# Kernel tuning notes

Measured on AMD Instinct MI355X. Metric: run time of the kernel, lower is better.

## Reference

```python
import jax, jax.numpy as jnp
import numpy as np

BETA_2 = 1.0
LAMBDA_2 = 1.0


def _segment_logsumexp(x, seg, num_segments):
    # numerically stable segment logsumexp; empty segments -> 0.0
    m = jax.ops.segment_max(x, seg, num_segments=num_segments)
    m_safe = jnp.where(jnp.isfinite(m), m, 0.0)
    s = jax.ops.segment_sum(jnp.exp(x - m_safe[seg]), seg, num_segments=num_segments)
    lse = m_safe + jnp.log(s)
    return jnp.where(s > 0, lse, 0.0)


def setup_inputs() -> dict:
    key = jax.random.key(0)
    k1, k2, k3, k4, k5 = jax.random.split(key, 5)
    num_nodes, d, num_edges, num_graphs = 100000, 64, 3200000, 256
    Q2 = jax.random.normal(k1, (num_nodes, d), dtype=jnp.float32)
    K2 = jax.random.normal(k2, (num_nodes, d), dtype=jnp.float32)
    c_2 = jax.random.randint(k3, (num_edges,), 0, num_nodes)
    u_2 = jax.random.randint(k4, (num_edges,), 0, num_nodes)
    batch = jnp.sort(jax.random.randint(k5, (num_nodes,), 0, num_graphs))
    return {"Q2": Q2, "K2": K2, "c_2": c_2, "u_2": u_2, "batch": batch,
            "num_graphs": num_graphs}


def reference(Q2, K2, c_2, u_2, batch, num_graphs):
    num_nodes, d = Q2.shape
    scale = d ** 0.5
    # pairwise dot over edges: [E]
    ell_2 = jnp.sum(Q2[c_2] * K2[u_2], axis=-1) / scale
    # segment logsumexp grouped by destination node c: [N]
    lse_2 = _segment_logsumexp(BETA_2 * ell_2, c_2, num_nodes)
    # scatter-add per-node lse into per-graph energy: [G]
    graph_lse = jax.ops.segment_sum(lse_2, batch, num_segments=num_graphs)
    E = (LAMBDA_2 / BETA_2) * graph_lse
    return E
```

## Files before the change

kernel.cpp:

```cpp
#include <hip/hip_runtime.h>
#include <hip/hip_fp8.h>
#include <math.h>

typedef __attribute__((ext_vector_type(2))) float fv2;

#if defined(__has_builtin)
#  if __has_builtin(__builtin_amdgcn_cvt_pk_f32_fp8) && \
      __has_builtin(__builtin_amdgcn_cvt_pk_fp8_f32)
#    define PE_HAVE_FP8_BUILTINS 1
#  endif
#endif

#define MAX_NB 1024
#define NPB 256
#define NPB_SHIFT 8
#define B2_EPT 16
#define B2_CHUNK (B2_EPT * 256)
#define CPB 4
#define RT 1024
#define NXCD 8

__device__ __forceinline__ unsigned pack4_fp8(float a, float b, float c, float d) {
#ifdef PE_HAVE_FP8_BUILTINS
    int w = 0;
    w = __builtin_amdgcn_cvt_pk_fp8_f32(a, b, w, false);
    w = __builtin_amdgcn_cvt_pk_fp8_f32(c, d, w, true);
    return (unsigned)w;
#else
    unsigned r = 0;
    r |= (unsigned)__hip_fp8_e4m3(a).__x;
    r |= (unsigned)__hip_fp8_e4m3(b).__x << 8;
    r |= (unsigned)__hip_fp8_e4m3(c).__x << 16;
    r |= (unsigned)__hip_fp8_e4m3(d).__x << 24;
    return r;
#endif
}

__device__ __forceinline__ float dot4w_fp8(unsigned qa, unsigned ka, float acc) {
#ifdef PE_HAVE_FP8_BUILTINS
    fv2 q0 = __builtin_amdgcn_cvt_pk_f32_fp8((int)qa, false);
    fv2 q1 = __builtin_amdgcn_cvt_pk_f32_fp8((int)qa, true);
    fv2 k0 = __builtin_amdgcn_cvt_pk_f32_fp8((int)ka, false);
    fv2 k1 = __builtin_amdgcn_cvt_pk_f32_fp8((int)ka, true);
    acc = fmaf(q0.x, k0.x, acc);
    acc = fmaf(q0.y, k0.y, acc);
    acc = fmaf(q1.x, k1.x, acc);
    acc = fmaf(q1.y, k1.y, acc);
    return acc;
#else
#pragma unroll
    for (int j = 0; j < 4; ++j) {
        __hip_fp8_e4m3 qv, kv;
        qv.__x = (qa >> (8 * j)) & 0xff;
        kv.__x = (ka >> (8 * j)) & 0xff;
        acc = fmaf((float)qv, (float)kv, acc);
    }
    return acc;
#endif
}

__device__ __forceinline__ float dot16_fp8(const uint4& q, const uint4& k) {
    float d = 0.0f;
    d = dot4w_fp8(q.x, k.x, d);
    d = dot4w_fp8(q.y, k.y, d);
    d = dot4w_fp8(q.z, k.z, d);
    d = dot4w_fp8(q.w, k.w, d);
    return d;
}

__device__ __forceinline__ float red4(float d) {
    d += __shfl_xor(d, 1, 64);
    d += __shfl_xor(d, 2, 64);
    return d;
}

__global__ __launch_bounds__(256) void pe_convert_kernel(
    const float* __restrict__ Q,
    const float* __restrict__ K,
    unsigned* __restrict__ Qq,
    unsigned* __restrict__ Kq,
    float* __restrict__ node_sum,
    float* __restrict__ out,
    int n4,
    int num_nodes,
    int num_graphs) {
    const int i = blockIdx.x * blockDim.x + threadIdx.x;
    if (i < num_nodes) node_sum[i] = 0.0f;
    if (i < num_graphs) out[i] = 0.0f;
    if (i >= n4) return;

    const float4 q = ((const float4*)Q)[i];
    const float4 k = ((const float4*)K)[i];
    Qq[i] = pack4_fp8(q.x, q.y, q.z, q.w);
    Kq[i] = pack4_fp8(k.x, k.y, k.z, k.w);
}

__global__ __launch_bounds__(256) void pe_count_kernel(
    const int* __restrict__ c,
    unsigned* __restrict__ cnt_mat,
    int num_edges, int nb, int nblk) {
    __shared__ unsigned h[MAX_NB];
    const int tid = threadIdx.x;
    const int blk = blockIdx.x;
    for (int b = tid; b < nb; b += 256) h[b] = 0u;
    __syncthreads();

    const int estart = blk * B2_CHUNK;
    const int ecount = min(B2_CHUNK, num_edges - estart);
    const int n4 = ecount >> 2;
    const int4* c4 = (const int4*)(c + estart);
    for (int k = tid; k < n4; k += 256) {
        const int4 v = c4[k];
        atomicAdd(&h[v.x >> NPB_SHIFT], 1u);
        atomicAdd(&h[v.y >> NPB_SHIFT], 1u);
        atomicAdd(&h[v.z >> NPB_SHIFT], 1u);
        atomicAdd(&h[v.w >> NPB_SHIFT], 1u);
    }
    for (int e = (n4 << 2) + tid; e < ecount; e += 256)
        atomicAdd(&h[c[estart + e] >> NPB_SHIFT], 1u);
    __syncthreads();

    for (int b = tid; b < nb; b += 256)
        cnt_mat[(size_t)b * nblk + blk] = h[b];
}

__global__ __launch_bounds__(256) void pe_matscan_kernel(
    unsigned* __restrict__ cnt_mat,
    unsigned* __restrict__ bucket_cnt,
    int nblk) {
    __shared__ unsigned s[256];
    const int t = threadIdx.x;
    unsigned* row = cnt_mat + (size_t)blockIdx.x * nblk;
    unsigned carry = 0u;
    for (int t0 = 0; t0 < nblk; t0 += 256) {
        const int i = t0 + t;
        const unsigned v = (i < nblk) ? row[i] : 0u;
        s[t] = v;
        __syncthreads();
        for (int off = 1; off < 256; off <<= 1) {
            const unsigned mine = s[t];
            const unsigned add = (t >= off) ? s[t - off] : 0u;
            __syncthreads();
            s[t] = mine + add;
            __syncthreads();
        }
        if (i < nblk) row[i] = carry + (s[t] - v);
        carry += s[255];
        __syncthreads();
    }
    if (t == 0) bucket_cnt[blockIdx.x] = carry;
}

__global__ __launch_bounds__(1024) void pe_scan_kernel(
    const unsigned* __restrict__ bucket_cnt,
    unsigned* __restrict__ bucket_base,
    int nb) {
    __shared__ unsigned s[MAX_NB];
    const int t = threadIdx.x;
    const unsigned v = (t < nb) ? bucket_cnt[t] : 0u;
    s[t] = v;
    __syncthreads();
    for (int off = 1; off < MAX_NB; off <<= 1) {
        const unsigned mine = s[t];
        const unsigned add = (t >= off) ? s[t - off] : 0u;
        __syncthreads();
        s[t] = mine + add;
        __syncthreads();
    }
    if (t < nb) bucket_base[t] = s[t] - v;
    if (t == 0) bucket_base[nb] = s[MAX_NB - 1];
}

__global__ __launch_bounds__(256) void pe_binify_kernel(
    const int* __restrict__ c,
    const int* __restrict__ u,
    const unsigned* __restrict__ cnt_mat,
    const unsigned* __restrict__ bucket_base,
    unsigned* __restrict__ recs,
    int num_edges, int nb, int nblk) {
    __shared__ unsigned rank[MAX_NB];
    __shared__ unsigned lstart[MAX_NB];
    __shared__ unsigned basesh[MAX_NB];
    __shared__ unsigned srec[B2_CHUNK];
    __shared__ unsigned short sbuk[B2_CHUNK];
    __shared__ unsigned wtot[4];

    const int tid = threadIdx.x;
    const int blk = blockIdx.x;
    const int estart = blk * B2_CHUNK;
    const int ecount = min(B2_CHUNK, num_edges - estart);

    for (int b = tid; b < MAX_NB; b += 256) rank[b] = 0u;
    for (int b = tid; b < nb; b += 256)
        basesh[b] = bucket_base[b] + cnt_mat[(size_t)b * nblk + blk];
    __syncthreads();

    unsigned rw[B2_EPT];
    int rb[B2_EPT];
    unsigned rr[B2_EPT];

    if (ecount == B2_CHUNK) {
        const int4* c4 = (const int4*)(c + estart);
        const int4* u4 = (const int4*)(u + estart);
#pragma unroll
        for (int jj = 0; jj < 4; ++jj) {
            const int k = jj * 256 + tid;
            const int4 cv = c4[k];
            const int4 uv = u4[k];
            const int j = jj * 4;
            rb[j + 0] = cv.x >> NPB_SHIFT;
            rb[j + 1] = cv.y >> NPB_SHIFT;
            rb[j + 2] = cv.z >> NPB_SHIFT;
            rb[j + 3] = cv.w >> NPB_SHIFT;
            rw[j + 0] = ((unsigned)uv.x << NPB_SHIFT) | (unsigned)(cv.x & (NPB - 1));
            rw[j + 1] = ((unsigned)uv.y << NPB_SHIFT) | (unsigned)(cv.y & (NPB - 1));
            rw[j + 2] = ((unsigned)uv.z << NPB_SHIFT) | (unsigned)(cv.z & (NPB - 1));
            rw[j + 3] = ((unsigned)uv.w << NPB_SHIFT) | (unsigned)(cv.w & (NPB - 1));
            rr[j + 0] = atomicAdd(&rank[rb[j + 0]], 1u);
            rr[j + 1] = atomicAdd(&rank[rb[j + 1]], 1u);
            rr[j + 2] = atomicAdd(&rank[rb[j + 2]], 1u);
            rr[j + 3] = atomicAdd(&rank[rb[j + 3]], 1u);
        }
    } else {
#pragma unroll
        for (int j = 0; j < B2_EPT; ++j) {
            rb[j] = -1;
            const int e = estart + j * 256 + tid;
            if (e < num_edges) {
                const int cc = c[e];
                const int uu = u[e];
                rb[j] = cc >> NPB_SHIFT;
                rw[j] = ((unsigned)uu << NPB_SHIFT) | (unsigned)(cc & (NPB - 1));
                rr[j] = atomicAdd(&rank[rb[j]], 1u);
            }
        }
    }
    __syncthreads();

    {
        const int b4 = tid * 4;
        const unsigned v0 = rank[b4 + 0];
        const unsigned v1 = rank[b4 + 1];
        const unsigned v2 = rank[b4 + 2];
        const unsigned v3 = rank[b4 + 3];
        const unsigned tsum = v0 + v1 + v2 + v3;
        unsigned incl = tsum;
        const int lane = tid & 63;
#pragma unroll
        for (int off = 1; off < 64; off <<= 1) {
            const unsigned nv = __shfl_up(incl, off, 64);
            if (lane >= off) incl += nv;
        }
        if (lane == 63) wtot[tid >> 6] = incl;
        __syncthreads();
        unsigned woff = 0;
        const int w = tid >> 6;
        for (int i = 0; i < w; ++i) woff += wtot[i];
        const unsigned ebase = woff + incl - tsum;
        lstart[b4 + 0] = ebase;
        lstart[b4 + 1] = ebase + v0;
        lstart[b4 + 2] = ebase + v0 + v1;
        lstart[b4 + 3] = ebase + v0 + v1 + v2;
    }
    __syncthreads();

#pragma unroll
    for (int j = 0; j < B2_EPT; ++j) {
        if (rb[j] >= 0) {
            const unsigned pos = lstart[rb[j]] + rr[j];
            srec[pos] = rw[j];
            sbuk[pos] = (unsigned short)rb[j];
        }
    }
    __syncthreads();

    for (int i = tid; i < ecount; i += 256) {
        const int b = sbuk[i];
        recs[basesh[b] + (unsigned)i - lstart[b]] = srec[i];
    }
}

__global__ __launch_bounds__(256) void pe_dotred_kernel(
    const unsigned* __restrict__ Qq,
    const unsigned* __restrict__ Kq,
    const unsigned* __restrict__ recs,
    const unsigned* __restrict__ bucket_base,
    float* __restrict__ node_sum,
    int num_nodes, int nb) {
    __shared__ uint4 qlds[NPB * 4];
    __shared__ float acc[NPB];
    __shared__ unsigned rlds[RT];

    const int g = blockIdx.x;
    const int xcd = g & (NXCD - 1);
    const int slot = g >> 3;
    const int B = xcd + NXCD * (slot / CPB);
    const int chunk = slot - (slot / CPB) * CPB;
    if (B >= nb) return;

    const int t = threadIdx.x;
    const int gteam = t >> 2;
    const int sub = t & 3;
    const float inv_scale = 0.125f;

    const int nrows = min(NPB, num_nodes - B * NPB);
    const uint4* qsrc = (const uint4*)Qq + (size_t)B * NPB * 4;
    for (int i = t; i < nrows * 4; i += 256) qlds[i] = qsrc[i];
    acc[t] = 0.0f;

    const unsigned s0 = bucket_base[B];
    const unsigned len = bucket_base[B + 1] - s0;
    const unsigned r0 = s0 + (unsigned)(((unsigned long long)len * chunk) / CPB);
    const unsigned r1 = s0 + (unsigned)(((unsigned long long)len * (chunk + 1)) / CPB);

    for (unsigned t0 = r0; t0 < r1; t0 += RT) {
        const unsigned n = min((unsigned)RT, r1 - t0);
        __syncthreads();
        for (unsigned i = t; i < n; i += 256) rlds[i] = recs[t0 + i];
        __syncthreads();
        for (unsigned i = gteam; i < n; i += 64) {
            const unsigned rec = rlds[i];
            const unsigned uu = rec >> NPB_SHIFT;
            const unsigned local = rec & (NPB - 1);
            const uint4 k = *(const uint4*)(Kq + (size_t)uu * 16 + sub * 4);
            const uint4 q = qlds[local * 4 + sub];
            const float d = red4(dot16_fp8(q, k));
            if (sub == 0) atomicAdd(&acc[local], __expf(d * inv_scale));
        }
    }
    __syncthreads();

    if (t < nrows && acc[t] != 0.0f)
        atomicAdd(&node_sum[B * NPB + t], acc[t]);
}

__global__ __launch_bounds__(256) void pe_node_kernel(
    const float* __restrict__ node_sum,
    const int* __restrict__ batch,
    float* __restrict__ out,
    int num_nodes) {
    const int n = blockIdx.x * blockDim.x + threadIdx.x;
    const bool valid = (n < num_nodes);
    const int nc = valid ? n : (num_nodes - 1);

    const float s = valid ? node_sum[nc] : 0.0f;
    float lse = (s > 0.0f) ? logf(s) : 0.0f;
    if (!valid) lse = 0.0f;
    const int b = batch[nc];

    const int b0 = __shfl(b, 0, 64);
    const bool uniform = __all(b == b0);
    if (uniform) {
        lse += __shfl_xor(lse, 1, 64);
        lse += __shfl_xor(lse, 2, 64);
        lse += __shfl_xor(lse, 4, 64);
        lse += __shfl_xor(lse, 8, 64);
        lse += __shfl_xor(lse, 16, 64);
        lse += __shfl_xor(lse, 32, 64);
        if ((threadIdx.x & 63) == 0 && lse != 0.0f) {
            atomicAdd(&out[b0], lse);
        }
    } else {
        if (valid && lse != 0.0f) {
            atomicAdd(&out[b], lse);
        }
    }
}


__global__ __launch_bounds__(256) void pe_edge_kernel(
    const unsigned* __restrict__ Qq,
    const unsigned* __restrict__ Kq,
    const int* __restrict__ c,
    const int* __restrict__ u,
    float* __restrict__ node_sum,
    int num_edges) {
    const int tid = blockIdx.x * blockDim.x + threadIdx.x;
    const int group = tid >> 2;
    const int sub = tid & 3;
    const int ngroups = (gridDim.x * blockDim.x) >> 2;
    const float inv_scale = 0.125f;

    const int E4 = num_edges & ~3;

    for (int base = group * 4; base < E4; base += ngroups * 4) {
        const int4 ci = *(const int4*)(c + base);
        const int4 ui = *(const int4*)(u + base);

        const uint4 q0 = *(const uint4*)(Qq + (size_t)ci.x * 16 + sub * 4);
        const uint4 q1 = *(const uint4*)(Qq + (size_t)ci.y * 16 + sub * 4);
        const uint4 q2 = *(const uint4*)(Qq + (size_t)ci.z * 16 + sub * 4);
        const uint4 q3 = *(const uint4*)(Qq + (size_t)ci.w * 16 + sub * 4);
        const uint4 k0 = *(const uint4*)(Kq + (size_t)ui.x * 16 + sub * 4);
        const uint4 k1 = *(const uint4*)(Kq + (size_t)ui.y * 16 + sub * 4);
        const uint4 k2 = *(const uint4*)(Kq + (size_t)ui.z * 16 + sub * 4);
        const uint4 k3 = *(const uint4*)(Kq + (size_t)ui.w * 16 + sub * 4);

        float d0 = red4(dot16_fp8(q0, k0));
        float d1 = red4(dot16_fp8(q1, k1));
        float d2 = red4(dot16_fp8(q2, k2));
        float d3 = red4(dot16_fp8(q3, k3));

        const float dsel = (sub == 0) ? d0 : (sub == 1) ? d1 : (sub == 2) ? d2 : d3;
        const int csel = (sub == 0) ? ci.x : (sub == 1) ? ci.y : (sub == 2) ? ci.z : ci.w;
        atomicAdd(&node_sum[csel], __expf(dsel * inv_scale));
    }

    for (int e = E4 + group; e < num_edges; e += ngroups) {
        const int cc = c[e];
        const int uu = u[e];
        const uint4 q = *(const uint4*)(Qq + (size_t)cc * 16 + sub * 4);
        const uint4 k = *(const uint4*)(Kq + (size_t)uu * 16 + sub * 4);
        float d = red4(dot16_fp8(q, k));
        if (sub == 0) atomicAdd(&node_sum[cc], __expf(d * inv_scale));
    }
}

extern "C" void kernel_launch(void* const* d_in, const int* in_sizes, int n_in,
                              void* d_out, int out_size, void* d_ws, size_t ws_size,
                              hipStream_t stream) {
    const float* Q2 = (const float*)d_in[0];
    const float* K2 = (const float*)d_in[1];
    const int* c_2 = (const int*)d_in[2];
    const int* u_2 = (const int*)d_in[3];
    const int* batch = (const int*)d_in[4];

    const int num_nodes = in_sizes[4];
    const int num_edges = in_sizes[2];
    const int num_graphs = out_size;
    const int d = in_sizes[0] / num_nodes;
    const size_t row_elems = (size_t)num_nodes * d;
    const size_t row_bytes = row_elems;

    const int nb = (num_nodes + NPB - 1) >> NPB_SHIFT;
    const int nblk = (num_edges + B2_CHUNK - 1) / B2_CHUNK;

    unsigned* Qq = (unsigned*)d_ws;
    unsigned* Kq = Qq + row_bytes / 4;
    unsigned* meta = Kq + row_bytes / 4;
    unsigned* bucket_cnt = meta;
    unsigned* bucket_base = meta + MAX_NB;
    float* node_sum_b = (float*)(meta + 2 * MAX_NB + 16);
    const size_t ns_pad = ((size_t)num_nodes + 15) & ~(size_t)15;
    unsigned* recs = (unsigned*)node_sum_b + ns_pad;
    unsigned* cnt_mat = recs + num_edges;
    float* node_sum_f = (float*)meta;
    float* out = (float*)d_out;

    const size_t need_binned = row_bytes * 2 + (size_t)(2 * MAX_NB + 16) * 4 +
                               ns_pad * 4 + (size_t)num_edges * 4 +
                               (size_t)nb * nblk * 4;
    const bool use_binned = (nb <= MAX_NB) && (ws_size >= need_binned) &&
                            (d == 64) && (num_nodes <= (1 << 23));

    float* node_sum = use_binned ? node_sum_b : node_sum_f;

    {
        const int n4 = (int)(row_elems / 4);
        const int block = 256;
        const int grid = (n4 + block - 1) / block;
        pe_convert_kernel<<<grid, block, 0, stream>>>(
            Q2, K2, Qq, Kq, node_sum, out, n4, num_nodes, num_graphs);
    }

    if (use_binned) {
        pe_count_kernel<<<nblk, 256, 0, stream>>>(c_2, cnt_mat,
                                                  num_edges, nb, nblk);
        pe_matscan_kernel<<<nb, 256, 0, stream>>>(cnt_mat, bucket_cnt, nblk);
        pe_scan_kernel<<<1, 1024, 0, stream>>>(bucket_cnt, bucket_base, nb);
        pe_binify_kernel<<<nblk, 256, 0, stream>>>(c_2, u_2, cnt_mat,
                                                   bucket_base, recs,
                                                   num_edges, nb, nblk);
        {
            const int grid = NXCD * ((nb + NXCD - 1) / NXCD) * CPB;
            pe_dotred_kernel<<<grid, 256, 0, stream>>>(Qq, Kq, recs,
                                                       bucket_base,
                                                       node_sum, num_nodes, nb);
        }
    } else {
        pe_edge_kernel<<<8192, 256, 0, stream>>>(Qq, Kq, c_2, u_2,
                                                 node_sum, num_edges);
    }

    {
        const int block = 256;
        const int grid = (num_nodes + block - 1) / block;
        pe_node_kernel<<<grid, block, 0, stream>>>(node_sum, batch, out,
                                                   num_nodes);
    }
}
```

Measured before the change: 197.8 us.

## Sub-bin edges by source-node quarter and fuse convert with count kernel

Each destination bucket is split into four sub-bins by which quarter of the node range the source index u falls in. Within a bucket, the dot-product kernel then walks edges grouped by u range, which should improve cache locality of K row gathers. The FP8 conversion and the histogram count are merged into one launch, with block index deciding the role, to save a kernel launch and let the two overlap. In exchange the count matrix, scans and binify shared arrays get four times more bins, adding scan and shared-memory cost.

```diff
diff --git a/kernel.cpp b/kernel.cpp
--- a/kernel.cpp
+++ b/kernel.cpp
@@ -11,7 +11,9 @@
 #  endif
 #endif
 
-#define MAX_NB 1024
+#define MAX_NB 512
+#define MAX_NB2 2048
+#define UQ 4
 #define NPB 256
 #define NPB_SHIFT 8
 #define B2_EPT 16
@@ -74,59 +76,69 @@
     return d;
 }
 
-__global__ __launch_bounds__(256) void pe_convert_kernel(
+__device__ __forceinline__ int uquarter(int uu, int t1, int t2, int t3) {
+    return (uu >= t1) + (uu >= t2) + (uu >= t3);
+}
+
+__global__ __launch_bounds__(256) void pe_convcount_kernel(
     const float* __restrict__ Q,
     const float* __restrict__ K,
     unsigned* __restrict__ Qq,
     unsigned* __restrict__ Kq,
     float* __restrict__ node_sum,
     float* __restrict__ out,
-    int n4,
-    int num_nodes,
-    int num_graphs) {
-    const int i = blockIdx.x * blockDim.x + threadIdx.x;
-    if (i < num_nodes) node_sum[i] = 0.0f;
-    if (i < num_graphs) out[i] = 0.0f;
-    if (i >= n4) return;
-
-    const float4 q = ((const float4*)Q)[i];
-    const float4 k = ((const float4*)K)[i];
-    Qq[i] = pack4_fp8(q.x, q.y, q.z, q.w);
-    Kq[i] = pack4_fp8(k.x, k.y, k.z, k.w);
-}
-
-__global__ __launch_bounds__(256) void pe_count_kernel(
     const int* __restrict__ c,
+    const int* __restrict__ u,
     unsigned* __restrict__ cnt_mat,
-    int num_edges, int nb, int nblk) {
-    __shared__ unsigned h[MAX_NB];
+    int n4, int num_nodes, int num_graphs, int num_edges,
+    int nb2, int nblk, int nconv,
+    int t1, int t2, int t3) {
+    __shared__ unsigned h[MAX_NB2];
     const int tid = threadIdx.x;
-    const int blk = blockIdx.x;
-    for (int b = tid; b < nb; b += 256) h[b] = 0u;
+
+    if (blockIdx.x < nconv) {
+        const int i = blockIdx.x * 256 + tid;
+        if (i < num_nodes) node_sum[i] = 0.0f;
+        if (i < num_graphs) out[i] = 0.0f;
+        if (i >= n4) return;
+        const float4 q = ((const float4*)Q)[i];
+        const float4 k = ((const float4*)K)[i];
+        Qq[i] = pack4_fp8(q.x, q.y, q.z, q.w);
+        Kq[i] = pack4_fp8(k.x, k.y, k.z, k.w);
+        return;
+    }
+
+    const int blk = blockIdx.x - nconv;
+    for (int b = tid; b < nb2; b += 256) h[b] = 0u;
     __syncthreads();
 
     const int estart = blk * B2_CHUNK;
     const int ecount = min(B2_CHUNK, num_edges - estart);
-    const int n4 = ecount >> 2;
+    const int n4e = ecount >> 2;
     const int4* c4 = (const int4*)(c + estart);
-    for (int k = tid; k < n4; k += 256) {
-        const int4 v = c4[k];
-        atomicAdd(&h[v.x >> NPB_SHIFT], 1u);
-        atomicAdd(&h[v.y >> NPB_SHIFT], 1u);
-        atomicAdd(&h[v.z >> NPB_SHIFT], 1u);
-        atomicAdd(&h[v.w >> NPB_SHIFT], 1u);
-    }
-    for (int e = (n4 << 2) + tid; e < ecount; e += 256)
-        atomicAdd(&h[c[estart + e] >> NPB_SHIFT], 1u);
-    __syncthreads();
-
-    for (int b = tid; b < nb; b += 256)
+    const int4* u4 = (const int4*)(u + estart);
+    for (int k = tid; k < n4e; k += 256) {
+        const int4 cv = c4[k];
+        const int4 uv = u4[k];
+        atomicAdd(&h[(cv.x >> NPB_SHIFT) * UQ + uquarter(uv.x, t1, t2, t3)], 1u);
+        atomicAdd(&h[(cv.y >> NPB_SHIFT) * UQ + uquarter(uv.y, t1, t2, t3)], 1u);
+        atomicAdd(&h[(cv.z >> NPB_SHIFT) * UQ + uquarter(uv.z, t1, t2, t3)], 1u);
+        atomicAdd(&h[(cv.w >> NPB_SHIFT) * UQ + uquarter(uv.w, t1, t2, t3)], 1u);
+    }
+    for (int e = (n4e << 2) + tid; e < ecount; e += 256) {
+        const int cc = c[estart + e];
+        const int uu = u[estart + e];
+        atomicAdd(&h[(cc >> NPB_SHIFT) * UQ + uquarter(uu, t1, t2, t3)], 1u);
+    }
+    __syncthreads();
+
+    for (int b = tid; b < nb2; b += 256)
         cnt_mat[(size_t)b * nblk + blk] = h[b];
 }
 
 __global__ __launch_bounds__(256) void pe_matscan_kernel(
     unsigned* __restrict__ cnt_mat,
-    unsigned* __restrict__ bucket_cnt,
+    unsigned* __restrict__ bin_cnt,
     int nblk) {
     __shared__ unsigned s[256];
     const int t = threadIdx.x;
@@ -148,39 +160,45 @@
         carry += s[255];
         __syncthreads();
     }
-    if (t == 0) bucket_cnt[blockIdx.x] = carry;
+    if (t == 0) bin_cnt[blockIdx.x] = carry;
 }
 
 __global__ __launch_bounds__(1024) void pe_scan_kernel(
-    const unsigned* __restrict__ bucket_cnt,
-    unsigned* __restrict__ bucket_base,
-    int nb) {
-    __shared__ unsigned s[MAX_NB];
+    const unsigned* __restrict__ bin_cnt,
+    unsigned* __restrict__ bin_base,
+    int nb2) {
+    __shared__ unsigned s[1024];
     const int t = threadIdx.x;
-    const unsigned v = (t < nb) ? bucket_cnt[t] : 0u;
-    s[t] = v;
-    __syncthreads();
-    for (int off = 1; off < MAX_NB; off <<= 1) {
+    const int i0 = 2 * t, i1 = 2 * t + 1;
+    const unsigned v0 = (i0 < nb2) ? bin_cnt[i0] : 0u;
+    const unsigned v1 = (i1 < nb2) ? bin_cnt[i1] : 0u;
+    const unsigned p = v0 + v1;
+    s[t] = p;
+    __syncthreads();
+    for (int off = 1; off < 1024; off <<= 1) {
         const unsigned mine = s[t];
         const unsigned add = (t >= off) ? s[t - off] : 0u;
         __syncthreads();
         s[t] = mine + add;
         __syncthreads();
     }
-    if (t < nb) bucket_base[t] = s[t] - v;
-    if (t == 0) bucket_base[nb] = s[MAX_NB - 1];
+    const unsigned excl = s[t] - p;
+    if (i0 < nb2) bin_base[i0] = excl;
+    if (i1 < nb2) bin_base[i1] = excl + v0;
+    if (t == 1023) bin_base[nb2] = s[1023];
 }
 
 __global__ __launch_bounds__(256) void pe_binify_kernel(
     const int* __restrict__ c,
     const int* __restrict__ u,
     const unsigned* __restrict__ cnt_mat,
-    const unsigned* __restrict__ bucket_base,
+    const unsigned* __restrict__ bin_base,
     unsigned* __restrict__ recs,
-    int num_edges, int nb, int nblk) {
-    __shared__ unsigned rank[MAX_NB];
-    __shared__ unsigned lstart[MAX_NB];
-    __shared__ unsigned basesh[MAX_NB];
+    int num_edges, int nb2, int nblk,
+    int t1, int t2, int t3) {
+    __shared__ unsigned rank[MAX_NB2];
+    __shared__ unsigned lstart[MAX_NB2];
+    __shared__ unsigned basesh[MAX_NB2];
     __shared__ unsigned srec[B2_CHUNK];
     __shared__ unsigned short sbuk[B2_CHUNK];
     __shared__ unsigned wtot[4];
@@ -190,9 +208,9 @@
     const int estart = blk * B2_CHUNK;
     const int ecount = min(B2_CHUNK, num_edges - estart);
 
-    for (int b = tid; b < MAX_NB; b += 256) rank[b] = 0u;
-    for (int b = tid; b < nb; b += 256)
-        basesh[b] = bucket_base[b] + cnt_mat[(size_t)b * nblk + blk];
+    for (int b = tid; b < MAX_NB2; b += 256) rank[b] = 0u;
+    for (int b = tid; b < nb2; b += 256)
+        basesh[b] = bin_base[b] + cnt_mat[(size_t)b * nblk + blk];
     __syncthreads();
 
     unsigned rw[B2_EPT];
@@ -208,10 +226,10 @@
             const int4 cv = c4[k];
             const int4 uv = u4[k];
             const int j = jj * 4;
-            rb[j + 0] = cv.x >> NPB_SHIFT;
-            rb[j + 1] = cv.y >> NPB_SHIFT;
-            rb[j + 2] = cv.z >> NPB_SHIFT;
-            rb[j + 3] = cv.w >> NPB_SHIFT;
+            rb[j + 0] = (cv.x >> NPB_SHIFT) * UQ + uquarter(uv.x, t1, t2, t3);
+            rb[j + 1] = (cv.y >> NPB_SHIFT) * UQ + uquarter(uv.y, t1, t2, t3);
+            rb[j + 2] = (cv.z >> NPB_SHIFT) * UQ + uquarter(uv.z, t1, t2, t3);
+            rb[j + 3] = (cv.w >> NPB_SHIFT) * UQ + uquarter(uv.w, t1, t2, t3);
             rw[j + 0] = ((unsigned)uv.x << NPB_SHIFT) | (unsigned)(cv.x & (NPB - 1));
             rw[j + 1] = ((unsigned)uv.y << NPB_SHIFT) | (unsigned)(cv.y & (NPB - 1));
             rw[j + 2] = ((unsigned)uv.z << NPB_SHIFT) | (unsigned)(cv.z & (NPB - 1));
@@ -229,7 +247,7 @@
             if (e < num_edges) {
                 const int cc = c[e];
                 const int uu = u[e];
-                rb[j] = cc >> NPB_SHIFT;
+                rb[j] = (cc >> NPB_SHIFT) * UQ + uquarter(uu, t1, t2, t3);
                 rw[j] = ((unsigned)uu << NPB_SHIFT) | (unsigned)(cc & (NPB - 1));
                 rr[j] = atomicAdd(&rank[rb[j]], 1u);
             }
@@ -238,12 +256,11 @@
     __syncthreads();
 
     {
-        const int b4 = tid * 4;
-        const unsigned v0 = rank[b4 + 0];
-        const unsigned v1 = rank[b4 + 1];
-        const unsigned v2 = rank[b4 + 2];
-        const unsigned v3 = rank[b4 + 3];
-        const unsigned tsum = v0 + v1 + v2 + v3;
+        const int b8 = tid * 8;
+        unsigned v[8];
+        unsigned tsum = 0;
+#pragma unroll
+        for (int i = 0; i < 8; ++i) { v[i] = rank[b8 + i]; tsum += v[i]; }
         unsigned incl = tsum;
         const int lane = tid & 63;
 #pragma unroll
@@ -256,11 +273,9 @@
         unsigned woff = 0;
         const int w = tid >> 6;
         for (int i = 0; i < w; ++i) woff += wtot[i];
-        const unsigned ebase = woff + incl - tsum;
-        lstart[b4 + 0] = ebase;
-        lstart[b4 + 1] = ebase + v0;
-        lstart[b4 + 2] = ebase + v0 + v1;
-        lstart[b4 + 3] = ebase + v0 + v1 + v2;
+        unsigned run = woff + incl - tsum;
+#pragma unroll
+        for (int i = 0; i < 8; ++i) { lstart[b8 + i] = run; run += v[i]; }
     }
     __syncthreads();
 
@@ -284,7 +299,7 @@
     const unsigned* __restrict__ Qq,
     const unsigned* __restrict__ Kq,
     const unsigned* __restrict__ recs,
-    const unsigned* __restrict__ bucket_base,
+    const unsigned* __restrict__ bin_base,
     float* __restrict__ node_sum,
     int num_nodes, int nb) {
     __shared__ uint4 qlds[NPB * 4];
@@ -308,8 +323,8 @@
     for (int i = t; i < nrows * 4; i += 256) qlds[i] = qsrc[i];
     acc[t] = 0.0f;
 
-    const unsigned s0 = bucket_base[B];
-    const unsigned len = bucket_base[B + 1] - s0;
+    const unsigned s0 = bin_base[B * UQ];
+    const unsigned len = bin_base[B * UQ + UQ] - s0;
     const unsigned r0 = s0 + (unsigned)(((unsigned long long)len * chunk) / CPB);
     const unsigned r1 = s0 + (unsigned)(((unsigned long long)len * (chunk + 1)) / CPB);
 
@@ -367,6 +382,24 @@
     }
 }
 
+
+__global__ __launch_bounds__(256) void pe_convert_kernel(
+    const float* __restrict__ Q,
+    const float* __restrict__ K,
+    unsigned* __restrict__ Qq,
+    unsigned* __restrict__ Kq,
+    float* __restrict__ node_sum,
+    float* __restrict__ out,
+    int n4, int num_nodes, int num_graphs) {
+    const int i = blockIdx.x * blockDim.x + threadIdx.x;
+    if (i < num_nodes) node_sum[i] = 0.0f;
+    if (i < num_graphs) out[i] = 0.0f;
+    if (i >= n4) return;
+    const float4 q = ((const float4*)Q)[i];
+    const float4 k = ((const float4*)K)[i];
+    Qq[i] = pack4_fp8(q.x, q.y, q.z, q.w);
+    Kq[i] = pack4_fp8(k.x, k.y, k.z, k.w);
+}
 
 __global__ __launch_bounds__(256) void pe_edge_kernel(
     const unsigned* __restrict__ Qq,
@@ -433,51 +466,55 @@
     const size_t row_bytes = row_elems;
 
     const int nb = (num_nodes + NPB - 1) >> NPB_SHIFT;
+    const int nb2 = nb * UQ;
     const int nblk = (num_edges + B2_CHUNK - 1) / B2_CHUNK;
+
+    const int t1 = num_nodes >> 2;
+    const int t2 = num_nodes >> 1;
+    const int t3 = t1 + t2;
 
     unsigned* Qq = (unsigned*)d_ws;
     unsigned* Kq = Qq + row_bytes / 4;
     unsigned* meta = Kq + row_bytes / 4;
-    unsigned* bucket_cnt = meta;
-    unsigned* bucket_base = meta + MAX_NB;
-    float* node_sum_b = (float*)(meta + 2 * MAX_NB + 16);
+    unsigned* bin_cnt = meta;
+    unsigned* bin_base = meta + MAX_NB2;
+    float* node_sum_b = (float*)(meta + 2 * MAX_NB2 + 16);
     const size_t ns_pad = ((size_t)num_nodes + 15) & ~(size_t)15;
     unsigned* recs = (unsigned*)node_sum_b + ns_pad;
     unsigned* cnt_mat = recs + num_edges;
     float* node_sum_f = (float*)meta;
     float* out = (float*)d_out;
 
-    const size_t need_binned = row_bytes * 2 + (size_t)(2 * MAX_NB + 16) * 4 +
+    const size_t need_binned = row_bytes * 2 + (size_t)(2 * MAX_NB2 + 16) * 4 +
                                ns_pad * 4 + (size_t)num_edges * 4 +
-                               (size_t)nb * nblk * 4;
+                               (size_t)nb2 * nblk * 4;
     const bool use_binned = (nb <= MAX_NB) && (ws_size >= need_binned) &&
                             (d == 64) && (num_nodes <= (1 << 23));
 
     float* node_sum = use_binned ? node_sum_b : node_sum_f;
-
-    {
-        const int n4 = (int)(row_elems / 4);
-        const int block = 256;
-        const int grid = (n4 + block - 1) / block;
-        pe_convert_kernel<<<grid, block, 0, stream>>>(
-            Q2, K2, Qq, Kq, node_sum, out, n4, num_nodes, num_graphs);
-    }
+    const int n4 = (int)(row_elems / 4);
+    const int nconv = (n4 + 255) / 256;
 
     if (use_binned) {
-        pe_count_kernel<<<nblk, 256, 0, stream>>>(c_2, cnt_mat,
-                                                  num_edges, nb, nblk);
-        pe_matscan_kernel<<<nb, 256, 0, stream>>>(cnt_mat, bucket_cnt, nblk);
-        pe_scan_kernel<<<1, 1024, 0, stream>>>(bucket_cnt, bucket_base, nb);
+        pe_convcount_kernel<<<nconv + nblk, 256, 0, stream>>>(
+            Q2, K2, Qq, Kq, node_sum, out, c_2, u_2, cnt_mat,
+            n4, num_nodes, num_graphs, num_edges, nb2, nblk, nconv,
+            t1, t2, t3);
+        pe_matscan_kernel<<<nb2, 256, 0, stream>>>(cnt_mat, bin_cnt, nblk);
+        pe_scan_kernel<<<1, 1024, 0, stream>>>(bin_cnt, bin_base, nb2);
         pe_binify_kernel<<<nblk, 256, 0, stream>>>(c_2, u_2, cnt_mat,
-                                                   bucket_base, recs,
-                                                   num_edges, nb, nblk);
+                                                   bin_base, recs,
+                                                   num_edges, nb2, nblk,
+                                                   t1, t2, t3);
         {
             const int grid = NXCD * ((nb + NXCD - 1) / NXCD) * CPB;
             pe_dotred_kernel<<<grid, 256, 0, stream>>>(Qq, Kq, recs,
-                                                       bucket_base,
+                                                       bin_base,
                                                        node_sum, num_nodes, nb);
         }
     } else {
+        pe_convert_kernel<<<nconv, 256, 0, stream>>>(
+            Q2, K2, Qq, Kq, node_sum, out, n4, num_nodes, num_graphs);
         pe_edge_kernel<<<8192, 256, 0, stream>>>(Qq, Kq, c_2, u_2,
                                                  node_sum, num_edges);
     }
```

Measured after the change: 236.8 us. 19.8% more time.
